# Optimization experiments

Measured on AMD Instinct MI355X. Metric: run time of the kernel, lower is better.

Reference implementation:

```python
import jax, jax.numpy as jnp
import numpy as np

B, S, H, MODES = 16, 8192, 256, 16

def setup_inputs() -> dict:
    key = jax.random.key(0)
    k1, k2, k3 = jax.random.split(key, 3)
    x = jax.random.normal(k1, (B, S, H), dtype=jnp.float32)
    # complex weights ~ 0.02 * randn (real and imag parts kept as floats)
    w_real = jax.random.normal(k2, (H, H, MODES), dtype=jnp.float32) * 0.02
    w_imag = jax.random.normal(k3, (H, H, MODES), dtype=jnp.float32) * 0.02
    return {"x": x, "w_real": w_real, "w_imag": w_imag}

def reference(x, w_real, w_imag):
    batch, seq_len, hidden = x.shape
    x_ft = jnp.fft.rfft(x, axis=1)                      # [B, F, H] complex64, F = S//2 + 1
    m = min(MODES, x_ft.shape[1])
    w = (w_real + 1j * w_imag)[:, :, :m]                # [H, K, m]
    # batched complex matmul over the kept modes (replaces per-mode loop)
    out_modes = jnp.einsum('bmh,hkm->bmk', x_ft[:, :m, :], w)
    out_ft = jnp.zeros_like(x_ft).at[:, :m, :].set(out_modes)
    y = jnp.fft.irfft(out_ft, n=seq_len, axis=1)        # [B, S, H] float32
    return jax.nn.gelu(y, approximate=False)            # torch nn.GELU default = exact erf
```

## Files before the change

kernel.cpp:

```cpp
#include <hip/hip_runtime.h>
#include <math.h>

#define BB 16
#define SS 8192
#define HH 256
#define MM 16
#define NV 2049
#define DCH 32
#define DNC 65
#define SCH 16
#define SNC 129


__global__ __launch_bounds__(256) void k_twiddle(float* __restrict__ T) {
    int idx = blockIdx.x * 256 + threadIdx.x;
    if (idx >= NV * MM) return;
    int v = idx >> 4, k = idx & 15;
    int r = (k * v) & (SS - 1);
    float th = (float)r * (6.28318530717958647692f / (float)SS);
    float sn, cn;
    sincosf(th, &sn, &cn);
    T[v * 32 + 2 * k]     = cn;
    T[v * 32 + 2 * k + 1] = sn;
}

__global__ __launch_bounds__(256) void k_wt(const float* __restrict__ wr,
                                            const float* __restrict__ wi,
                                            float* __restrict__ Wtr,
                                            float* __restrict__ Wti) {
    __shared__ float lds[4096 + 256];
    const int h = blockIdx.x, t = threadIdx.x;
    const float* src = (blockIdx.y == 0 ? wr : wi) + (size_t)h * 4096;
    float* dst = (blockIdx.y == 0 ? Wtr : Wti);
#pragma unroll
    for (int j = 0; j < 16; j++) {
        int i = j * 256 + t;
        lds[i + (i >> 4)] = src[i];
    }
    __syncthreads();
#pragma unroll
    for (int m = 0; m < 16; m++) {
        int i = t * 16 + m;
        dst[(size_t)m * (HH * HH) + (size_t)h * HH + t] = lds[i + (i >> 4)];
    }
}

__device__ __forceinline__ float fast_gelu(float y) {
    float x  = fabsf(y) * 0.70710678118654752f;
    float t  = __builtin_amdgcn_rcpf(fmaf(0.3275911f, x, 1.0f));
    float e  = __expf(-x * x);
    float p  = fmaf(fmaf(fmaf(fmaf(1.061405429f, t, -1.453152027f), t,
                   1.421413741f), t, -0.284496736f), t, 0.254829592f) * t;
    float erfabs = fmaf(-p, e, 1.0f);
    return fmaf(0.5f * fabsf(y), erfabs, 0.5f * y);
}

__global__ __launch_bounds__(256) void k_dft(const float* __restrict__ x,
                                             const float* __restrict__ T,
                                             float* __restrict__ Xp) {
    const int c = blockIdx.x, b = blockIdx.y, h = threadIdx.x;
    float cs[MM], sn[MM];
#pragma unroll
    for (int k = 0; k < MM; k++) { cs[k] = 0.f; sn[k] = 0.f; }

    const int nv = (c == DNC - 1) ? 1 : DCH;
    const int v0 = c * DCH;
    const float* xb = x + (size_t)b * SS * HH + h;

#pragma unroll 2
    for (int i = 0; i < nv; i++) {
        int v = v0 + i;
        float hf = (v == 0 || v == SS / 4) ? 0.5f : 1.0f;
        float x0 = xb[(size_t)v * HH];
        float x1 = xb[(size_t)((SS - v) & (SS - 1)) * HH];
        float x2 = xb[(size_t)(SS / 2 - v) * HH];
        float x3 = xb[(size_t)(SS / 2 + v) * HH];
        float u = (x0 + x1) * hf, d = (x0 - x1) * hf;
        float w = (x2 + x3) * hf, e = (x3 - x2) * hf;
        float upw = u + w, umw = u - w, dpe = d + e, dme = d - e;
        const float4* tw4 = (const float4*)(T + (size_t)v * 32);
#pragma unroll
        for (int j = 0; j < 8; j++) {
            float4 t = tw4[j];
            cs[2 * j]     = fmaf(t.x, upw, cs[2 * j]);
            sn[2 * j]     = fmaf(t.y, dpe, sn[2 * j]);
            cs[2 * j + 1] = fmaf(t.z, umw, cs[2 * j + 1]);
            sn[2 * j + 1] = fmaf(t.w, dme, sn[2 * j + 1]);
        }
    }

    size_t base = ((size_t)(b * DNC + c) * MM) * (2 * HH) + h;
#pragma unroll
    for (int k = 0; k < MM; k++) {
        Xp[base + (size_t)k * (2 * HH)]      = cs[k];
        Xp[base + (size_t)k * (2 * HH) + HH] = sn[k];
    }
}

__global__ __launch_bounds__(256) void k_reduce(const float* __restrict__ Xp,
                                                float* __restrict__ Xs) {
    const int t = blockIdx.x * 256 + threadIdx.x;
    const int INNER = MM * 2 * HH;
    int idx4 = t * 4;
    int inner = idx4 & (INNER - 1);
    int b = idx4 >> 13;
    const float* src = Xp + ((size_t)b * DNC) * INNER + inner;
    float4 s = make_float4(0.f, 0.f, 0.f, 0.f);
#pragma unroll 5
    for (int p = 0; p < DNC; p++) {
        float4 v = *(const float4*)(src + (size_t)p * INNER);
        s.x += v.x; s.y += v.y; s.z += v.z; s.w += v.w;
    }
    *(float4*)(Xs + idx4) = s;
}

__global__ __launch_bounds__(256) void k_mix2(const float* __restrict__ Xs,
                                              const float* __restrict__ Wtr,
                                              const float* __restrict__ Wti,
                                              float* __restrict__ AB) {
    const int m = blockIdx.x, b = blockIdx.y, t = threadIdx.x;
    __shared__ float xr_s[HH], xs_s[HH];
    size_t xbase = (((size_t)b * MM + m) * 2) * HH;
    xr_s[t] = Xs[xbase + t];
    xs_s[t] = Xs[xbase + HH + t];
    __syncthreads();

    const float* wr_m = Wtr + (size_t)m * (HH * HH);
    const float* wi_m = Wti + (size_t)m * (HH * HH);
    float re = 0.f, im = 0.f;
#pragma unroll 8
    for (int h = 0; h < HH; h++) {
        float a  = wr_m[(size_t)h * HH + t];
        float bw = wi_m[(size_t)h * HH + t];
        float xr = xr_s[h];
        float xs = xs_s[h];
        re = fmaf(xr, a, re);  re = fmaf(xs, bw, re);
        im = fmaf(xr, bw, im); im = fmaf(-xs, a, im);
    }
    float scale = (m == 0 ? 1.f : 2.f) / (float)SS;
    size_t o = (((size_t)b * MM + m) * 2) * HH + t;
    AB[o]      = scale * re;
    AB[o + HH] = -scale * im;
}

__global__ __launch_bounds__(256) void k_synth(const float* __restrict__ AB,
                                               const float* __restrict__ T,
                                               float* __restrict__ out) {
    const int c = blockIdx.x, b = blockIdx.y, h = threadIdx.x;
    float a[MM], bc[MM];
#pragma unroll
    for (int k = 0; k < MM; k++) {
        size_t o = (((size_t)b * MM + k) * 2) * HH + h;
        a[k]  = AB[o];
        bc[k] = AB[o + HH];
    }
    const int nv = (c == SNC - 1) ? 1 : SCH;
    const int v0 = c * SCH;
    float* ob = out + (size_t)b * SS * HH + h;

#pragma unroll 2
    for (int i = 0; i < nv; i++) {
        int v = v0 + i;
        const float4* tw4 = (const float4*)(T + (size_t)v * 32);
        float Pe = 0.f, Po = 0.f, Qe = 0.f, Qo = 0.f;
#pragma unroll
        for (int j = 0; j < 8; j++) {
            float4 t = tw4[j];
            Pe = fmaf(a[2 * j],      t.x, Pe);
            Qe = fmaf(bc[2 * j],     t.y, Qe);
            Po = fmaf(a[2 * j + 1],  t.z, Po);
            Qo = fmaf(bc[2 * j + 1], t.w, Qo);
        }
        float Pp = Pe + Po, Pm = Pe - Po, Qp = Qe + Qo, Qm = Qe - Qo;
        ob[(size_t)v * HH]                        = fast_gelu(Pp + Qp);
        ob[(size_t)(SS / 2 - v) * HH]             = fast_gelu(Pm - Qm);
        ob[(size_t)(SS / 2 + v) * HH]             = fast_gelu(Pm + Qm);
        ob[(size_t)((SS - v) & (SS - 1)) * HH]    = fast_gelu(Pp - Qp);
    }
}

extern "C" void kernel_launch(void* const* d_in, const int* in_sizes, int n_in,
                              void* d_out, int out_size, void* d_ws, size_t ws_size,
                              hipStream_t stream) {
    const float* x   = (const float*)d_in[0];
    const float* w_r = (const float*)d_in[1];
    const float* w_i = (const float*)d_in[2];
    float* out = (float*)d_out;
    float* ws  = (float*)d_ws;

    float* T   = ws;
    float* AB  = ws + 262144;
    float* Xs  = ws + 393216;
    float* Xp  = out;
    float* Wtr = out + (size_t)16 * 1024 * 1024;
    float* Wti = out + (size_t)17 * 1024 * 1024;

    hipLaunchKernelGGL(k_twiddle, dim3((NV * MM + 255) / 256), dim3(256), 0, stream, T);
    hipLaunchKernelGGL(k_wt,     dim3(HH, 2), dim3(256), 0, stream, w_r, w_i, Wtr, Wti);
    hipLaunchKernelGGL(k_dft,    dim3(DNC, BB), dim3(256), 0, stream, x, T, Xp);
    hipLaunchKernelGGL(k_reduce, dim3(BB * MM * 2 * HH / 1024), dim3(256), 0, stream, Xp, Xs);
    hipLaunchKernelGGL(k_mix2,   dim3(MM, BB), dim3(256), 0, stream, Xs, Wtr, Wti, AB);
    hipLaunchKernelGGL(k_synth,  dim3(SNC, BB), dim3(256), 0, stream, AB, T, out);
}
```

Baseline: 117.2 us.

## Double-buffer DFT input rows into LDS with async global_load_lds

Restructures the forward DFT kernel so that each block streams its four mirrored row groups (v, S/2-v, S/2+v, S-v) into a double-buffered LDS tile using asynchronous global-to-LDS loads. Explicit vmcnt waits and barriers let the next chunk load while the current one is computed. This is meant to hide global memory latency behind the twiddle FMAs. The v=0 term moves into a dedicated last block. The cost is 64KB of LDS per block, which may limit occupancy, plus extra barriers.

Measured after the change: 117.0 us. No clear change (-0.2%).

```diff
diff --git a/kernel.cpp b/kernel.cpp
--- a/kernel.cpp
+++ b/kernel.cpp
@@ -6,11 +6,18 @@
 #define HH 256
 #define MM 16
 #define NV 2049
-#define DCH 32
+#define VC 8
+#define CPB 4
 #define DNC 65
 #define SCH 16
 #define SNC 129
 
+
+__device__ __forceinline__ void gl_lds16(const float* g, float* l) {
+    __builtin_amdgcn_global_load_lds(
+        (const __attribute__((address_space(1))) void*)g,
+        (__attribute__((address_space(3))) void*)l, 16, 0, 0);
+}
 
 __global__ __launch_bounds__(256) void k_twiddle(float* __restrict__ T) {
     int idx = blockIdx.x * 256 + threadIdx.x;
@@ -58,38 +65,84 @@
 __global__ __launch_bounds__(256) void k_dft(const float* __restrict__ x,
                                              const float* __restrict__ T,
                                              float* __restrict__ Xp) {
-    const int c = blockIdx.x, b = blockIdx.y, h = threadIdx.x;
+    const int b = blockIdx.y, bx = blockIdx.x, t = threadIdx.x;
+    const int w = t >> 6;
+    const float* xb = x + (size_t)b * SS * HH;
+
     float cs[MM], sn[MM];
 #pragma unroll
     for (int k = 0; k < MM; k++) { cs[k] = 0.f; sn[k] = 0.f; }
 
-    const int nv = (c == DNC - 1) ? 1 : DCH;
-    const int v0 = c * DCH;
-    const float* xb = x + (size_t)b * SS * HH + h;
-
-#pragma unroll 2
-    for (int i = 0; i < nv; i++) {
-        int v = v0 + i;
-        float hf = (v == 0 || v == SS / 4) ? 0.5f : 1.0f;
-        float x0 = xb[(size_t)v * HH];
-        float x1 = xb[(size_t)((SS - v) & (SS - 1)) * HH];
-        float x2 = xb[(size_t)(SS / 2 - v) * HH];
-        float x3 = xb[(size_t)(SS / 2 + v) * HH];
-        float u = (x0 + x1) * hf, d = (x0 - x1) * hf;
-        float w = (x2 + x3) * hf, e = (x3 - x2) * hf;
-        float upw = u + w, umw = u - w, dpe = d + e, dme = d - e;
-        const float4* tw4 = (const float4*)(T + (size_t)v * 32);
+    __shared__ float lds[2][4 * VC * HH];
+
+    if (bx == 64) {
+        float x0 = xb[t];
+        float x2 = xb[(size_t)(SS / 2) * HH + t];
 #pragma unroll
         for (int j = 0; j < 8; j++) {
-            float4 t = tw4[j];
-            cs[2 * j]     = fmaf(t.x, upw, cs[2 * j]);
-            sn[2 * j]     = fmaf(t.y, dpe, sn[2 * j]);
-            cs[2 * j + 1] = fmaf(t.z, umw, cs[2 * j + 1]);
-            sn[2 * j + 1] = fmaf(t.w, dme, sn[2 * j + 1]);
+            cs[2 * j]     = x0 + x2;
+            cs[2 * j + 1] = x0 - x2;
         }
-    }
-
-    size_t base = ((size_t)(b * DNC + c) * MM) * (2 * HH) + h;
+    } else {
+        const int c0 = bx * CPB;
+
+        auto stage = [&](int c, int buf) {
+            int v0 = 1 + VC * c;
+            const float* bases[4] = {
+                xb + (size_t)v0 * HH,
+                xb + (size_t)(SS / 2 - v0 - (VC - 1)) * HH,
+                xb + (size_t)(SS / 2 + v0) * HH,
+                xb + (size_t)(SS - v0 - (VC - 1)) * HH };
+#pragma unroll
+            for (int s = 0; s < 4; s++)
+#pragma unroll
+                for (int q = 0; q < 2; q++)
+                    gl_lds16(bases[s] + q * 1024 + t * 4,
+                             &lds[buf][s * 2048 + q * 1024 + w * 256]);
+        };
+
+        auto compute = [&](int c, int buf) {
+            int v0 = 1 + VC * c;
+            const float* L = &lds[buf][0];
+#pragma unroll
+            for (int i = 0; i < VC; i++) {
+                int v = v0 + i;
+                float x0 = L[0 * 2048 + i * 256 + t];
+                float x2 = L[1 * 2048 + (VC - 1 - i) * 256 + t];
+                float x3 = L[2 * 2048 + i * 256 + t];
+                float x1 = L[3 * 2048 + (VC - 1 - i) * 256 + t];
+                float hf = (v == SS / 4) ? 0.5f : 1.0f;
+                float u = (x0 + x1) * hf, d = (x0 - x1) * hf;
+                float ww = (x2 + x3) * hf, e = (x3 - x2) * hf;
+                float upw = u + ww, umw = u - ww, dpe = d + e, dme = d - e;
+                const float4* tw4 = (const float4*)(T + (size_t)v * 32);
+#pragma unroll
+                for (int j = 0; j < 8; j++) {
+                    float4 tt = tw4[j];
+                    cs[2 * j]     = fmaf(tt.x, upw, cs[2 * j]);
+                    sn[2 * j]     = fmaf(tt.y, dpe, sn[2 * j]);
+                    cs[2 * j + 1] = fmaf(tt.z, umw, cs[2 * j + 1]);
+                    sn[2 * j + 1] = fmaf(tt.w, dme, sn[2 * j + 1]);
+                }
+            }
+        };
+
+        stage(c0, 0);
+        for (int j = 0; j < CPB; j++) {
+            if (j < CPB - 1) {
+                stage(c0 + j + 1, (j + 1) & 1);
+                asm volatile("s_waitcnt vmcnt(8)" ::: "memory");
+            } else {
+                asm volatile("s_waitcnt vmcnt(0)" ::: "memory");
+            }
+            __builtin_amdgcn_sched_barrier(0);
+            __builtin_amdgcn_s_barrier();
+            compute(c0 + j, j & 1);
+            __builtin_amdgcn_s_barrier();
+        }
+    }
+
+    size_t base = ((size_t)(b * DNC + bx) * MM) * (2 * HH) + t;
 #pragma unroll
     for (int k = 0; k < MM; k++) {
         Xp[base + (size_t)k * (2 * HH)]      = cs[k];
```

## Merge setup kernels, fuse partial-sum reduction into mix, simplify DFT symmetry

Applied to the files above, without the earlier changes.

Combines the twiddle-table and weight-transpose kernels into one launch, and folds the separate partial-sum reduction into the mode-mixing kernel. The mixing is now split into two halves over the hidden dimension, and the synthesis kernel sums the two halves. The forward DFT switches from four-way to two-way symmetry over a larger twiddle table, using 32 chunks of 128 rows. This removes two launches and a round trip through global memory for the reduction. In exchange the DFT does more FMAs and twiddle reads per input element, and its grid is about half as many blocks, which may hide memory latency less well.

Measured after the change: 118.4 us. No clear change (+1.0%).

```diff
diff --git a/kernel.cpp b/kernel.cpp
--- a/kernel.cpp
+++ b/kernel.cpp
@@ -5,43 +5,45 @@
 #define SS 8192
 #define HH 256
 #define MM 16
-#define NV 2049
-#define DCH 32
-#define DNC 65
+#define DNC 32
+#define DL 128
 #define SCH 16
 #define SNC 129
+#define QOFF (BB * MM * 2 * HH)
 
 
-__global__ __launch_bounds__(256) void k_twiddle(float* __restrict__ T) {
-    int idx = blockIdx.x * 256 + threadIdx.x;
-    if (idx >= NV * MM) return;
-    int v = idx >> 4, k = idx & 15;
-    int r = (k * v) & (SS - 1);
-    float th = (float)r * (6.28318530717958647692f / (float)SS);
-    float sn, cn;
-    sincosf(th, &sn, &cn);
-    T[v * 32 + 2 * k]     = cn;
-    T[v * 32 + 2 * k + 1] = sn;
-}
-
-__global__ __launch_bounds__(256) void k_wt(const float* __restrict__ wr,
-                                            const float* __restrict__ wi,
-                                            float* __restrict__ Wtr,
-                                            float* __restrict__ Wti) {
-    __shared__ float lds[4096 + 256];
-    const int h = blockIdx.x, t = threadIdx.x;
-    const float* src = (blockIdx.y == 0 ? wr : wi) + (size_t)h * 4096;
-    float* dst = (blockIdx.y == 0 ? Wtr : Wti);
+__global__ __launch_bounds__(256) void k_pre(const float* __restrict__ wr,
+                                             const float* __restrict__ wi,
+                                             float* __restrict__ T2,
+                                             float* __restrict__ Wtr,
+                                             float* __restrict__ Wti) {
+    const int t = threadIdx.x;
+    if (blockIdx.x < 256) {
+        int idx = blockIdx.x * 256 + t;
+        int s = idx >> 4, k = idx & 15;
+        int r = (k * s) & (SS - 1);
+        float th = (float)r * (6.28318530717958647692f / (float)SS);
+        float sn, cn;
+        sincosf(th, &sn, &cn);
+        T2[s * 32 + 2 * k]     = cn;
+        T2[s * 32 + 2 * k + 1] = sn;
+    } else {
+        __shared__ float lds[4096 + 256];
+        int bid = blockIdx.x - 256;
+        int h = bid & 255, y = bid >> 8;
+        const float* src = (y == 0 ? wr : wi) + (size_t)h * 4096;
+        float* dst = (y == 0 ? Wtr : Wti);
 #pragma unroll
-    for (int j = 0; j < 16; j++) {
-        int i = j * 256 + t;
-        lds[i + (i >> 4)] = src[i];
-    }
-    __syncthreads();
+        for (int j = 0; j < 16; j++) {
+            int i = j * 256 + t;
+            lds[i + (i >> 4)] = src[i];
+        }
+        __syncthreads();
 #pragma unroll
-    for (int m = 0; m < 16; m++) {
-        int i = t * 16 + m;
-        dst[(size_t)m * (HH * HH) + (size_t)h * HH + t] = lds[i + (i >> 4)];
+        for (int m = 0; m < 16; m++) {
+            int i = t * 16 + m;
+            dst[(size_t)m * (HH * HH) + (size_t)h * HH + t] = lds[i + (i >> 4)];
+        }
     }
 }
 
@@ -56,40 +58,35 @@
 }
 
 __global__ __launch_bounds__(256) void k_dft(const float* __restrict__ x,
-                                             const float* __restrict__ T,
+                                             const float* __restrict__ T2,
                                              float* __restrict__ Xp) {
-    const int c = blockIdx.x, b = blockIdx.y, h = threadIdx.x;
+    const int c = blockIdx.x, b = blockIdx.y, t = threadIdx.x;
+    const int s0 = c * DL;
+    const float* x0 = x + (size_t)b * SS * HH + (size_t)s0 * HH + t;
+    const float* x1 = x0 + (size_t)(SS / 2) * HH;
+    const float* tw = T2 + (size_t)s0 * 32;
+
     float cs[MM], sn[MM];
 #pragma unroll
     for (int k = 0; k < MM; k++) { cs[k] = 0.f; sn[k] = 0.f; }
 
-    const int nv = (c == DNC - 1) ? 1 : DCH;
-    const int v0 = c * DCH;
-    const float* xb = x + (size_t)b * SS * HH + h;
-
-#pragma unroll 2
-    for (int i = 0; i < nv; i++) {
-        int v = v0 + i;
-        float hf = (v == 0 || v == SS / 4) ? 0.5f : 1.0f;
-        float x0 = xb[(size_t)v * HH];
-        float x1 = xb[(size_t)((SS - v) & (SS - 1)) * HH];
-        float x2 = xb[(size_t)(SS / 2 - v) * HH];
-        float x3 = xb[(size_t)(SS / 2 + v) * HH];
-        float u = (x0 + x1) * hf, d = (x0 - x1) * hf;
-        float w = (x2 + x3) * hf, e = (x3 - x2) * hf;
-        float upw = u + w, umw = u - w, dpe = d + e, dme = d - e;
-        const float4* tw4 = (const float4*)(T + (size_t)v * 32);
+#pragma unroll 4
+    for (int i = 0; i < DL; i++) {
+        float xa = x0[(size_t)i * HH];
+        float xb = x1[(size_t)i * HH];
+        float u = xa + xb, d = xa - xb;
+        const float4* t4 = (const float4*)(tw + (size_t)i * 32);
 #pragma unroll
         for (int j = 0; j < 8; j++) {
-            float4 t = tw4[j];
-            cs[2 * j]     = fmaf(t.x, upw, cs[2 * j]);
-            sn[2 * j]     = fmaf(t.y, dpe, sn[2 * j]);
-            cs[2 * j + 1] = fmaf(t.z, umw, cs[2 * j + 1]);
-            sn[2 * j + 1] = fmaf(t.w, dme, sn[2 * j + 1]);
+            float4 tt = t4[j];
+            cs[2 * j]     = fmaf(tt.x, u, cs[2 * j]);
+            sn[2 * j]     = fmaf(tt.y, u, sn[2 * j]);
+            cs[2 * j + 1] = fmaf(tt.z, d, cs[2 * j + 1]);
+            sn[2 * j + 1] = fmaf(tt.w, d, sn[2 * j + 1]);
         }
     }
 
-    size_t base = ((size_t)(b * DNC + c) * MM) * (2 * HH) + h;
+    size_t base = ((size_t)(b * DNC + c) * MM) * (2 * HH) + t;
 #pragma unroll
     for (int k = 0; k < MM; k++) {
         Xp[base + (size_t)k * (2 * HH)]      = cs[k];
@@ -97,62 +94,63 @@
     }
 }
 
-__global__ __launch_bounds__(256) void k_reduce(const float* __restrict__ Xp,
-                                                float* __restrict__ Xs) {
-    const int t = blockIdx.x * 256 + threadIdx.x;
-    const int INNER = MM * 2 * HH;
-    int idx4 = t * 4;
-    int inner = idx4 & (INNER - 1);
-    int b = idx4 >> 13;
-    const float* src = Xp + ((size_t)b * DNC) * INNER + inner;
-    float4 s = make_float4(0.f, 0.f, 0.f, 0.f);
-#pragma unroll 5
-    for (int p = 0; p < DNC; p++) {
-        float4 v = *(const float4*)(src + (size_t)p * INNER);
-        s.x += v.x; s.y += v.y; s.z += v.z; s.w += v.w;
+__global__ __launch_bounds__(256) void k_mix(const float* __restrict__ Xp,
+                                             const float* __restrict__ Wtr,
+                                             const float* __restrict__ Wti,
+                                             float* __restrict__ ABp) {
+    const int m = blockIdx.x, b = blockIdx.y, q = blockIdx.z, t = threadIdx.x;
+    const int h0 = q * 128;
+    __shared__ float tmp[2][2][128];
+    __shared__ float xr_s[128], xs_s[128];
+
+    {
+        int hh = t & 127, ph = t >> 7;
+        float s0 = 0.f, s1 = 0.f;
+        size_t base = (((size_t)b * DNC + ph * 16) * MM + m) * (2 * HH) + h0 + hh;
+        const size_t ps = (size_t)MM * 2 * HH;
+#pragma unroll 4
+        for (int p = 0; p < 16; p++) {
+            s0 += Xp[base + (size_t)p * ps];
+            s1 += Xp[base + (size_t)p * ps + HH];
+        }
+        tmp[ph][0][hh] = s0;
+        tmp[ph][1][hh] = s1;
+        __syncthreads();
+        if (t < 128) {
+            xr_s[t] = tmp[0][0][t] + tmp[1][0][t];
+            xs_s[t] = tmp[0][1][t] + tmp[1][1][t];
+        }
+        __syncthreads();
     }
-    *(float4*)(Xs + idx4) = s;
-}
 
-__global__ __launch_bounds__(256) void k_mix2(const float* __restrict__ Xs,
-                                              const float* __restrict__ Wtr,
-                                              const float* __restrict__ Wti,
-                                              float* __restrict__ AB) {
-    const int m = blockIdx.x, b = blockIdx.y, t = threadIdx.x;
-    __shared__ float xr_s[HH], xs_s[HH];
-    size_t xbase = (((size_t)b * MM + m) * 2) * HH;
-    xr_s[t] = Xs[xbase + t];
-    xs_s[t] = Xs[xbase + HH + t];
-    __syncthreads();
-
-    const float* wr_m = Wtr + (size_t)m * (HH * HH);
-    const float* wi_m = Wti + (size_t)m * (HH * HH);
+    const float* wr_m = Wtr + (size_t)m * (HH * HH) + (size_t)h0 * HH;
+    const float* wi_m = Wti + (size_t)m * (HH * HH) + (size_t)h0 * HH;
     float re = 0.f, im = 0.f;
 #pragma unroll 8
-    for (int h = 0; h < HH; h++) {
-        float a  = wr_m[(size_t)h * HH + t];
-        float bw = wi_m[(size_t)h * HH + t];
-        float xr = xr_s[h];
-        float xs = xs_s[h];
+    for (int hh = 0; hh < 128; hh++) {
+        float a  = wr_m[(size_t)hh * HH + t];
+        float bw = wi_m[(size_t)hh * HH + t];
+        float xr = xr_s[hh];
+        float xs = xs_s[hh];
         re = fmaf(xr, a, re);  re = fmaf(xs, bw, re);
         im = fmaf(xr, bw, im); im = fmaf(-xs, a, im);
     }
     float scale = (m == 0 ? 1.f : 2.f) / (float)SS;
-    size_t o = (((size_t)b * MM + m) * 2) * HH + t;
-    AB[o]      = scale * re;
-    AB[o + HH] = -scale * im;
+    size_t o = (size_t)q * QOFF + (((size_t)b * MM + m) * 2) * HH + t;
+    ABp[o]      = scale * re;
+    ABp[o + HH] = -scale * im;
 }
 
-__global__ __launch_bounds__(256) void k_synth(const float* __restrict__ AB,
-                                               const float* __restrict__ T,
+__global__ __launch_bounds__(256) void k_synth(const float* __restrict__ ABp,
+                                               const float* __restrict__ T2,
                                                float* __restrict__ out) {
     const int c = blockIdx.x, b = blockIdx.y, h = threadIdx.x;
     float a[MM], bc[MM];
 #pragma unroll
     for (int k = 0; k < MM; k++) {
         size_t o = (((size_t)b * MM + k) * 2) * HH + h;
-        a[k]  = AB[o];
-        bc[k] = AB[o + HH];
+        a[k]  = ABp[o]      + ABp[o + QOFF];
+        bc[k] = ABp[o + HH] + ABp[o + HH + QOFF];
     }
     const int nv = (c == SNC - 1) ? 1 : SCH;
     const int v0 = c * SCH;
@@ -161,7 +159,7 @@
 #pragma unroll 2
     for (int i = 0; i < nv; i++) {
         int v = v0 + i;
-        const float4* tw4 = (const float4*)(T + (size_t)v * 32);
+        const float4* tw4 = (const float4*)(T2 + (size_t)v * 32);
         float Pe = 0.f, Po = 0.f, Qe = 0.f, Qo = 0.f;
 #pragma unroll
         for (int j = 0; j < 8; j++) {
@@ -188,17 +186,14 @@
     float* out = (float*)d_out;
     float* ws  = (float*)d_ws;
 
-    float* T   = ws;
-    float* AB  = ws + 262144;
-    float* Xs  = ws + 393216;
+    float* T2  = ws;
+    float* ABp = ws + 131072;
     float* Xp  = out;
     float* Wtr = out + (size_t)16 * 1024 * 1024;
     float* Wti = out + (size_t)17 * 1024 * 1024;
 
-    hipLaunchKernelGGL(k_twiddle, dim3((NV * MM + 255) / 256), dim3(256), 0, stream, T);
-    hipLaunchKernelGGL(k_wt,     dim3(HH, 2), dim3(256), 0, stream, w_r, w_i, Wtr, Wti);
-    hipLaunchKernelGGL(k_dft,    dim3(DNC, BB), dim3(256), 0, stream, x, T, Xp);
-    hipLaunchKernelGGL(k_reduce, dim3(BB * MM * 2 * HH / 1024), dim3(256), 0, stream, Xp, Xs);
-    hipLaunchKernelGGL(k_mix2,   dim3(MM, BB), dim3(256), 0, stream, Xs, Wtr, Wti, AB);
-    hipLaunchKernelGGL(k_synth,  dim3(SNC, BB), dim3(256), 0, stream, AB, T, out);
+    hipLaunchKernelGGL(k_pre,   dim3(768), dim3(256), 0, stream, w_r, w_i, T2, Wtr, Wti);
+    hipLaunchKernelGGL(k_dft,   dim3(DNC, BB), dim3(256), 0, stream, x, T2, Xp);
+    hipLaunchKernelGGL(k_mix,   dim3(MM, BB, 2), dim3(256), 0, stream, Xp, Wtr, Wti, ABp);
+    hipLaunchKernelGGL(k_synth, dim3(SNC, BB), dim3(256), 0, stream, ABp, T2, out);
 }
```
